# Performance work log

Hardware: AMD Instinct MI355X
Metric: run time of the kernel (lower is better)

The kernel has to match this reference:

```python
import jax, jax.numpy as jnp
import numpy as np

CHANNELS = 10
LENGTH = 64
DEPTH = 4
BATCH = 2048


def setup_inputs() -> dict:
    key = jax.random.key(0)
    x = jax.random.normal(key, (BATCH, CHANNELS * LENGTH), dtype=jnp.float32)
    return {"x": x}


def _seg_exp(dx, depth):
    # Signature of a single linear segment with increment dx: (B, C).
    # Level k is dx^{(x)k} / k! (flattened to (B, C^k)).
    b = dx.shape[0]
    terms = [dx]
    for k in range(2, depth + 1):
        t = jnp.einsum('bi,bj->bij', terms[-1], dx).reshape(b, -1) / k
        terms.append(t)
    return tuple(terms)


def _chen(a, b, depth):
    # Truncated tensor-algebra product (Chen's identity), both with scalar part 1.
    # (A (x) B)_k = A_k + B_k + sum_{i=1}^{k-1} A_i (x) B_{k-i}
    bsz = a[0].shape[0]
    out = []
    for k in range(1, depth + 1):
        t = a[k - 1] + b[k - 1]
        for i in range(1, k):
            t = t + jnp.einsum('bi,bj->bij', a[i - 1], b[k - i - 1]).reshape(bsz, -1)
        out.append(t)
    return tuple(out)


def signature(path, depth):
    # path: (B, C, L). Increments along the path (last) dimension.
    dx = (path[:, :, 1:] - path[:, :, :-1]).transpose(0, 2, 1)  # (B, L-1, C)
    init = _seg_exp(dx[:, 0], depth)

    def step(carry, dxt):
        return _chen(carry, _seg_exp(dxt, depth), depth), None

    sig, _ = jax.lax.scan(step, init, dx[:, 1:].transpose(1, 0, 2))  # scan over L-2 steps
    return jnp.concatenate(sig, axis=-1)  # (B, sum_k C^k)


def reference(x):
    path = x.reshape(x.shape[0], CHANNELS, LENGTH)
    return signature(path, DEPTH)
```

## Files before the change

### kernel.cpp

```cpp
#include <hip/hip_runtime.h>
#include <hip/hip_bf16.h>


typedef short short8 __attribute__((ext_vector_type(8)));
typedef float f2 __attribute__((ext_vector_type(2)));
typedef float f32x4 __attribute__((ext_vector_type(4)));
typedef unsigned int uint4v __attribute__((ext_vector_type(4)));

constexpr int C = 10, L = 64, T = 63;
constexpr int OUTSZ = 10 + 100 + 1000 + 10000;
constexpr int DXP = 11;
constexpr int KS = 64;

__device__ __forceinline__ unsigned packbf(float lo, float hi) {
  union { __hip_bfloat162 h; unsigned u; } cv;
  cv.h = __float22bfloat162_rn(make_float2(lo, hi));
  return cv.u;
}
__device__ __forceinline__ int swz(int row, int k) {
  return row * KS + ((((k >> 3) ^ (row & 7)) << 3) | (k & 7));
}

__global__ __launch_bounds__(512, 6) void sig4_kernel(
    const float* __restrict__ x, float* __restrict__ out)
{
  __shared__ __align__(16) unsigned char smem_raw[45280];
  unsigned short* Ab = (unsigned short*)smem_raw;
  unsigned short* Ub = (unsigned short*)(smem_raw + 12800);
  unsigned short* Bb = (unsigned short*)(smem_raw + 25600);
  float* dxs = (float*)(smem_raw + 39680);
  float* Ps  = (float*)(smem_raw + 42452);

  const int t = threadIdx.x;
  const int w = t >> 6, lane = t & 63;
  const float* __restrict__ xb = x + (size_t)blockIdx.x * (C * L);
  float* __restrict__ ob = out + (size_t)blockIdx.x * OUTSZ;

  for (int i = t; i < T * C; i += 512) {
    int c = i / T, s = i - c * T;
    dxs[s * DXP + c] = xb[c * L + s + 1] - xb[c * L + s];
  }
  __syncthreads();
  for (int c = w; c < C; c += 8) {
    float v = (lane > 0) ? dxs[(lane - 1) * DXP + c] : 0.f;
    #pragma unroll
    for (int d = 1; d < 64; d <<= 1) {
      float y = __shfl_up(v, d);
      if (lane >= d) v += y;
    }
    Ps[lane * DXP + c] = v;
  }
  __syncthreads();

  if (t < 100) {
    const int i_ = t / 10, j_ = t - (t / 10) * 10;
    float s2 = 0.f;
    #pragma unroll
    for (int ch = 0; ch < 8; ++ch) {
      float bu[8], bv[8], zz[8];
      #pragma unroll
      for (int ee = 0; ee < 8; ++ee) {
        const int s = ch * 8 + ee;
        if (s < T) {
          float di = dxs[s * DXP + i_];
          float dj = dxs[s * DXP + j_];
          float p  = Ps[s * DXP + i_];
          bu[ee] = fmaf(di, 0.25f, p) * (dj * (1.f / 3.f));
          bv[ee] = fmaf(di, (1.f / 3.f), p) * (dj * 0.5f);
          zz[ee] = fmaf(di, 0.5f, p) * dj;
        } else { bu[ee] = 0.f; bv[ee] = 0.f; zz[ee] = 0.f; }
      }
      float u2v[8], v2v[8];
      #pragma unroll
      for (int ee = 0; ee < 8; ++ee) {
        u2v[ee] = bu[ee] + s2;
        v2v[ee] = bv[ee] + s2;
        s2 += zz[ee];
      }
      uint4v vp, up;
      #pragma unroll
      for (int q = 0; q < 4; ++q) {
        vp[q] = packbf(v2v[2 * q], v2v[2 * q + 1]);
        up[q] = packbf(u2v[2 * q], u2v[2 * q + 1]);
      }
      *(uint4v*)&Ab[swz(t, ch * 8)] = vp;
      *(uint4v*)&Ub[swz(t, ch * 8)] = up;
    }
    ob[10 + t] = s2;
    if (j_ == 0) ob[i_] = Ps[63 * DXP + i_];
  } else if (t >= 128) {
    const int q = t - 128;
    for (int task = q; task < 110 * 8; task += 384) {
      const int col = task >> 3, ch = task & 7;
      float b1v[8];
      if (col < 100) {
        const int k2 = col / 10, l2 = col - (col / 10) * 10;
        const float S1l = Ps[63 * DXP + l2];
        #pragma unroll
        for (int ee = 0; ee < 8; ++ee) {
          const int kk = ch * 8 + ee;
          b1v[ee] = (kk < T)
              ? dxs[kk * DXP + k2] * (S1l - Ps[(kk + 1) * DXP + l2]) : 0.f;
        }
      } else {
        const int c2 = col - 100;
        #pragma unroll
        for (int ee = 0; ee < 8; ++ee) {
          const int kk = ch * 8 + ee;
          b1v[ee] = (kk < T) ? dxs[kk * DXP + c2] : 0.f;
        }
      }
      uint4v pk;
      #pragma unroll
      for (int qq = 0; qq < 4; ++qq) pk[qq] = packbf(b1v[2 * qq], b1v[2 * qq + 1]);
      *(uint4v*)&Bb[swz(col, ch * 8)] = pk;
    }
  }
  __syncthreads();

  const int lm = lane & 15, lg = lane >> 4;
  f32x4 acc[7];
  #pragma unroll
  for (int ct = 0; ct < 7; ++ct) acc[ct] = f32x4{0.f, 0.f, 0.f, 0.f};

  if (w < 7) {
    const int arow = w * 16 + lm;
    short8 a0 = (arow < 100) ? *(const short8*)&Ab[swz(arow, lg * 8)]
                             : short8{0, 0, 0, 0, 0, 0, 0, 0};
    short8 a1 = (arow < 100) ? *(const short8*)&Ab[swz(arow, 32 + lg * 8)]
                             : short8{0, 0, 0, 0, 0, 0, 0, 0};
    #pragma unroll
    for (int ct = 0; ct < 7; ++ct) {
      const int bcol = ct * 16 + lm;
      short8 b0 = (bcol < 110) ? *(const short8*)&Bb[swz(bcol, lg * 8)]
                               : short8{0, 0, 0, 0, 0, 0, 0, 0};
      short8 b1 = (bcol < 110) ? *(const short8*)&Bb[swz(bcol, 32 + lg * 8)]
                               : short8{0, 0, 0, 0, 0, 0, 0, 0};
      acc[ct] = __builtin_amdgcn_mfma_f32_16x16x32_bf16(b0, a0, acc[ct], 0, 0, 0);
      acc[ct] = __builtin_amdgcn_mfma_f32_16x16x32_bf16(b1, a1, acc[ct], 0, 0, 0);
    }
  }
  __syncthreads();

  for (int task = t; task < 110 * 8; task += 512) {
    const int col = task >> 3, ch = task & 7;
    float b2v[8] = {0.f, 0.f, 0.f, 0.f, 0.f, 0.f, 0.f, 0.f};
    if (col < 100) {
      const int k2 = col / 10, l2 = col - (col / 10) * 10;
      #pragma unroll
      for (int ee = 0; ee < 8; ++ee) {
        const int kk = ch * 8 + ee;
        b2v[ee] = (kk < T) ? dxs[kk * DXP + k2] * dxs[kk * DXP + l2] * 0.5f : 0.f;
      }
    }
    uint4v pk;
    #pragma unroll
    for (int qq = 0; qq < 4; ++qq) pk[qq] = packbf(b2v[2 * qq], b2v[2 * qq + 1]);
    *(uint4v*)&Bb[swz(col, ch * 8)] = pk;
  }
  __syncthreads();

  if (w < 7) {
    const int arow = w * 16 + lm;
    short8 a0 = (arow < 100) ? *(const short8*)&Ub[swz(arow, lg * 8)]
                             : short8{0, 0, 0, 0, 0, 0, 0, 0};
    short8 a1 = (arow < 100) ? *(const short8*)&Ub[swz(arow, 32 + lg * 8)]
                             : short8{0, 0, 0, 0, 0, 0, 0, 0};
    #pragma unroll
    for (int ct = 0; ct < 7; ++ct) {
      const int bcol = ct * 16 + lm;
      short8 b0 = (bcol < 110) ? *(const short8*)&Bb[swz(bcol, lg * 8)]
                               : short8{0, 0, 0, 0, 0, 0, 0, 0};
      short8 b1 = (bcol < 110) ? *(const short8*)&Bb[swz(bcol, 32 + lg * 8)]
                               : short8{0, 0, 0, 0, 0, 0, 0, 0};
      acc[ct] = __builtin_amdgcn_mfma_f32_16x16x32_bf16(b0, a0, acc[ct], 0, 0, 0);
      acc[ct] = __builtin_amdgcn_mfma_f32_16x16x32_bf16(b1, a1, acc[ct], 0, 0, 0);
    }

    const int row = w * 16 + lm;
    if (row < 100) {
      float* rowp4 = ob + 1110 + row * 100;
      float* rowp3 = ob + 110 + row * 10;
      #pragma unroll
      for (int ct = 0; ct < 7; ++ct) {
        const int colbase = ct * 16 + lg * 4;
        f2 lo = {acc[ct][0], acc[ct][1]};
        f2 hi = {acc[ct][2], acc[ct][3]};
        if (colbase < 100) {
          *(f2*)(rowp4 + colbase) = lo;
          *(f2*)(rowp4 + colbase + 2) = hi;
        } else if (colbase < 110) {
          *(f2*)(rowp3 + (colbase - 100)) = lo;
          if (colbase < 108) *(f2*)(rowp3 + (colbase - 98)) = hi;
        }
      }
    }
  }
}

extern "C" void kernel_launch(void* const* d_in, const int* in_sizes, int n_in,
                              void* d_out, int out_size, void* d_ws, size_t ws_size,
                              hipStream_t stream) {
  const float* x = (const float*)d_in[0];
  float* out = (float*)d_out;
  const int batch = in_sizes[0] / (C * L);
  sig4_kernel<<<dim3(batch), dim3(512), 0, stream>>>(x, out);
}
```

Baseline: 35.93 us.

## Parallelize level-2 prefix computation across 8-lane groups with segmented shuffle scan

The serial per-row loop over 64 steps, run by only 100 threads, is split so that each of 8 lanes handles one 8-step chunk. Chunk offsets come from an 8-wide shuffle prefix sum. All 512 threads then share the A/U row building and the B1 column building, where before the threads were split into separate role groups. This shortens the critical path of the setup phase that the MFMA stage waits on, at the cost of extra shuffles and a different floating-point summation order.

```diff
diff --git a/kernel.cpp b/kernel.cpp
--- a/kernel.cpp
+++ b/kernel.cpp
@@ -52,30 +52,40 @@
   }
   __syncthreads();
 
-  if (t < 100) {
-    const int i_ = t / 10, j_ = t - (t / 10) * 10;
-    float s2 = 0.f;
-    #pragma unroll
-    for (int ch = 0; ch < 8; ++ch) {
-      float bu[8], bv[8], zz[8];
-      #pragma unroll
-      for (int ee = 0; ee < 8; ++ee) {
-        const int s = ch * 8 + ee;
+  const int g = lane & 7;
+  #pragma unroll 1
+  for (int it = 0; it < 2; ++it) {
+    const int row = it * 64 + w * 8 + (lane >> 3);
+    if (row < 100) {
+      const int i_ = row / 10, j_ = row - (row / 10) * 10;
+      float z[8], bu[8], bv[8];
+      #pragma unroll
+      for (int e = 0; e < 8; ++e) {
+        const int s = g * 8 + e;
         if (s < T) {
           float di = dxs[s * DXP + i_];
           float dj = dxs[s * DXP + j_];
           float p  = Ps[s * DXP + i_];
-          bu[ee] = fmaf(di, 0.25f, p) * (dj * (1.f / 3.f));
-          bv[ee] = fmaf(di, (1.f / 3.f), p) * (dj * 0.5f);
-          zz[ee] = fmaf(di, 0.5f, p) * dj;
-        } else { bu[ee] = 0.f; bv[ee] = 0.f; zz[ee] = 0.f; }
-      }
+          bu[e] = fmaf(di, 0.25f, p) * (dj * (1.f / 3.f));
+          bv[e] = fmaf(di, (1.f / 3.f), p) * (dj * 0.5f);
+          z[e]  = fmaf(di, 0.5f, p) * dj;
+        } else { bu[e] = 0.f; bv[e] = 0.f; z[e] = 0.f; }
+      }
+      float zsum = ((z[0] + z[1]) + (z[2] + z[3])) +
+                   ((z[4] + z[5]) + (z[6] + z[7]));
+      float a = zsum;
+      #pragma unroll
+      for (int d = 1; d < 8; d <<= 1) {
+        float y = __shfl_up(a, d, 8);
+        if (g >= d) a += y;
+      }
+      float s2 = a - zsum;
       float u2v[8], v2v[8];
       #pragma unroll
-      for (int ee = 0; ee < 8; ++ee) {
-        u2v[ee] = bu[ee] + s2;
-        v2v[ee] = bv[ee] + s2;
-        s2 += zz[ee];
+      for (int e = 0; e < 8; ++e) {
+        u2v[e] = bu[e] + s2;
+        v2v[e] = bv[e] + s2;
+        s2 += z[e];
       }
       uint4v vp, up;
       #pragma unroll
@@ -83,38 +93,37 @@
         vp[q] = packbf(v2v[2 * q], v2v[2 * q + 1]);
         up[q] = packbf(u2v[2 * q], u2v[2 * q + 1]);
       }
-      *(uint4v*)&Ab[swz(t, ch * 8)] = vp;
-      *(uint4v*)&Ub[swz(t, ch * 8)] = up;
-    }
-    ob[10 + t] = s2;
-    if (j_ == 0) ob[i_] = Ps[63 * DXP + i_];
-  } else if (t >= 128) {
-    const int q = t - 128;
-    for (int task = q; task < 110 * 8; task += 384) {
-      const int col = task >> 3, ch = task & 7;
-      float b1v[8];
-      if (col < 100) {
-        const int k2 = col / 10, l2 = col - (col / 10) * 10;
-        const float S1l = Ps[63 * DXP + l2];
-        #pragma unroll
-        for (int ee = 0; ee < 8; ++ee) {
-          const int kk = ch * 8 + ee;
-          b1v[ee] = (kk < T)
-              ? dxs[kk * DXP + k2] * (S1l - Ps[(kk + 1) * DXP + l2]) : 0.f;
-        }
-      } else {
-        const int c2 = col - 100;
-        #pragma unroll
-        for (int ee = 0; ee < 8; ++ee) {
-          const int kk = ch * 8 + ee;
-          b1v[ee] = (kk < T) ? dxs[kk * DXP + c2] : 0.f;
-        }
-      }
-      uint4v pk;
-      #pragma unroll
-      for (int qq = 0; qq < 4; ++qq) pk[qq] = packbf(b1v[2 * qq], b1v[2 * qq + 1]);
-      *(uint4v*)&Bb[swz(col, ch * 8)] = pk;
-    }
+      *(uint4v*)&Ab[swz(row, g * 8)] = vp;
+      *(uint4v*)&Ub[swz(row, g * 8)] = up;
+      if (g == 7) ob[10 + row] = s2;
+    }
+  }
+  if (t < 10) ob[t] = Ps[63 * DXP + t];
+
+  for (int task = t; task < 110 * 8; task += 512) {
+    const int col = task >> 3, ch = task & 7;
+    float b1v[8];
+    if (col < 100) {
+      const int k2 = col / 10, l2 = col - (col / 10) * 10;
+      const float S1l = Ps[63 * DXP + l2];
+      #pragma unroll
+      for (int ee = 0; ee < 8; ++ee) {
+        const int kk = ch * 8 + ee;
+        b1v[ee] = (kk < T)
+            ? dxs[kk * DXP + k2] * (S1l - Ps[(kk + 1) * DXP + l2]) : 0.f;
+      }
+    } else {
+      const int c2 = col - 100;
+      #pragma unroll
+      for (int ee = 0; ee < 8; ++ee) {
+        const int kk = ch * 8 + ee;
+        b1v[ee] = (kk < T) ? dxs[kk * DXP + c2] : 0.f;
+      }
+    }
+    uint4v pk;
+    #pragma unroll
+    for (int qq = 0; qq < 4; ++qq) pk[qq] = packbf(b1v[2 * qq], b1v[2 * qq + 1]);
+    *(uint4v*)&Bb[swz(col, ch * 8)] = pk;
   }
   __syncthreads();
 
```

After: 37.80 us. 5.2% more time.

## Transpose dx and prefix-sum scratch to channel-major padded layout for vector LDS loads

Applied to the files above, without the earlier changes.

Stores the path increments and their prefix sums in shared memory channel-major with a padded stride of 68 and explicit zero padding. The staging loops can then use 128-bit vector LDS reads and drop the per-element bounds checks. This is meant to cut scalar LDS instruction count and branch overhead in the operand-building phases. Vector loads at row strides of 68 floats may cause different bank-conflict patterns.

```diff
diff --git a/kernel.cpp b/kernel.cpp
--- a/kernel.cpp
+++ b/kernel.cpp
@@ -4,12 +4,13 @@
 
 typedef short short8 __attribute__((ext_vector_type(8)));
 typedef float f2 __attribute__((ext_vector_type(2)));
+typedef float f4 __attribute__((ext_vector_type(4)));
 typedef float f32x4 __attribute__((ext_vector_type(4)));
 typedef unsigned int uint4v __attribute__((ext_vector_type(4)));
 
 constexpr int C = 10, L = 64, T = 63;
 constexpr int OUTSZ = 10 + 100 + 1000 + 10000;
-constexpr int DXP = 11;
+constexpr int SP = 68;
 constexpr int KS = 64;
 
 __device__ __forceinline__ unsigned packbf(float lo, float hi) {
@@ -24,58 +25,64 @@
 __global__ __launch_bounds__(512, 6) void sig4_kernel(
     const float* __restrict__ x, float* __restrict__ out)
 {
-  __shared__ __align__(16) unsigned char smem_raw[45280];
+  __shared__ __align__(16) unsigned char smem_raw[45120];
   unsigned short* Ab = (unsigned short*)smem_raw;
   unsigned short* Ub = (unsigned short*)(smem_raw + 12800);
   unsigned short* Bb = (unsigned short*)(smem_raw + 25600);
-  float* dxs = (float*)(smem_raw + 39680);
-  float* Ps  = (float*)(smem_raw + 42452);
+  float* dxT = (float*)(smem_raw + 39680);
+  float* PsT = (float*)(smem_raw + 42400);
 
   const int t = threadIdx.x;
   const int w = t >> 6, lane = t & 63;
   const float* __restrict__ xb = x + (size_t)blockIdx.x * (C * L);
   float* __restrict__ ob = out + (size_t)blockIdx.x * OUTSZ;
 
-  for (int i = t; i < T * C; i += 512) {
-    int c = i / T, s = i - c * T;
-    dxs[s * DXP + c] = xb[c * L + s + 1] - xb[c * L + s];
+  for (int i = t; i < C * SP; i += 512) {
+    int c = i / SP, s = i - c * SP;
+    float v = 0.f;
+    if (s < T) v = xb[c * L + s + 1] - xb[c * L + s];
+    dxT[i] = v;
   }
   __syncthreads();
   for (int c = w; c < C; c += 8) {
-    float v = (lane > 0) ? dxs[(lane - 1) * DXP + c] : 0.f;
+    float v = (lane > 0) ? dxT[c * SP + lane - 1] : 0.f;
     #pragma unroll
     for (int d = 1; d < 64; d <<= 1) {
       float y = __shfl_up(v, d);
       if (lane >= d) v += y;
     }
-    Ps[lane * DXP + c] = v;
-  }
+    PsT[c * SP + lane] = v;
+  }
+  if (t < 40) PsT[(t >> 2) * SP + 64 + (t & 3)] = 0.f;
   __syncthreads();
 
   if (t < 100) {
     const int i_ = t / 10, j_ = t - (t / 10) * 10;
+    const float* dip = dxT + i_ * SP;
+    const float* pp  = PsT + i_ * SP;
+    const float* djp = dxT + j_ * SP;
     float s2 = 0.f;
     #pragma unroll
     for (int ch = 0; ch < 8; ++ch) {
+      f4 d0 = *(const f4*)(dip + ch * 8), d1 = *(const f4*)(dip + ch * 8 + 4);
+      f4 p0 = *(const f4*)(pp  + ch * 8), p1 = *(const f4*)(pp  + ch * 8 + 4);
+      f4 e0 = *(const f4*)(djp + ch * 8), e1 = *(const f4*)(djp + ch * 8 + 4);
+      float di[8] = {d0.x, d0.y, d0.z, d0.w, d1.x, d1.y, d1.z, d1.w};
+      float pv[8] = {p0.x, p0.y, p0.z, p0.w, p1.x, p1.y, p1.z, p1.w};
+      float dj[8] = {e0.x, e0.y, e0.z, e0.w, e1.x, e1.y, e1.z, e1.w};
       float bu[8], bv[8], zz[8];
       #pragma unroll
-      for (int ee = 0; ee < 8; ++ee) {
-        const int s = ch * 8 + ee;
-        if (s < T) {
-          float di = dxs[s * DXP + i_];
-          float dj = dxs[s * DXP + j_];
-          float p  = Ps[s * DXP + i_];
-          bu[ee] = fmaf(di, 0.25f, p) * (dj * (1.f / 3.f));
-          bv[ee] = fmaf(di, (1.f / 3.f), p) * (dj * 0.5f);
-          zz[ee] = fmaf(di, 0.5f, p) * dj;
-        } else { bu[ee] = 0.f; bv[ee] = 0.f; zz[ee] = 0.f; }
+      for (int e = 0; e < 8; ++e) {
+        bu[e] = fmaf(di[e], 0.25f, pv[e]) * (dj[e] * (1.f / 3.f));
+        bv[e] = fmaf(di[e], (1.f / 3.f), pv[e]) * (dj[e] * 0.5f);
+        zz[e] = fmaf(di[e], 0.5f, pv[e]) * dj[e];
       }
       float u2v[8], v2v[8];
       #pragma unroll
-      for (int ee = 0; ee < 8; ++ee) {
-        u2v[ee] = bu[ee] + s2;
-        v2v[ee] = bv[ee] + s2;
-        s2 += zz[ee];
+      for (int e = 0; e < 8; ++e) {
+        u2v[e] = bu[e] + s2;
+        v2v[e] = bv[e] + s2;
+        s2 += zz[e];
       }
       uint4v vp, up;
       #pragma unroll
@@ -87,33 +94,35 @@
       *(uint4v*)&Ub[swz(t, ch * 8)] = up;
     }
     ob[10 + t] = s2;
-    if (j_ == 0) ob[i_] = Ps[63 * DXP + i_];
+    if (j_ == 0) ob[i_] = PsT[i_ * SP + 63];
   } else if (t >= 128) {
     const int q = t - 128;
     for (int task = q; task < 110 * 8; task += 384) {
       const int col = task >> 3, ch = task & 7;
+      const int base = ch * 8;
       float b1v[8];
       if (col < 100) {
         const int k2 = col / 10, l2 = col - (col / 10) * 10;
-        const float S1l = Ps[63 * DXP + l2];
+        const float* dk = dxT + k2 * SP;
+        const float* pl = PsT + l2 * SP;
+        const float S1l = pl[63];
+        f4 d0 = *(const f4*)(dk + base), d1 = *(const f4*)(dk + base + 4);
+        f4 pa = *(const f4*)(pl + base), pb = *(const f4*)(pl + base + 4);
+        f4 pc = *(const f4*)(pl + base + 8);
+        float dv[8] = {d0.x, d0.y, d0.z, d0.w, d1.x, d1.y, d1.z, d1.w};
+        float Pn[8] = {pa.y, pa.z, pa.w, pb.x, pb.y, pb.z, pb.w, pc.x};
         #pragma unroll
-        for (int ee = 0; ee < 8; ++ee) {
-          const int kk = ch * 8 + ee;
-          b1v[ee] = (kk < T)
-              ? dxs[kk * DXP + k2] * (S1l - Ps[(kk + 1) * DXP + l2]) : 0.f;
-        }
+        for (int e = 0; e < 8; ++e) b1v[e] = dv[e] * (S1l - Pn[e]);
       } else {
-        const int c2 = col - 100;
-        #pragma unroll
-        for (int ee = 0; ee < 8; ++ee) {
-          const int kk = ch * 8 + ee;
-          b1v[ee] = (kk < T) ? dxs[kk * DXP + c2] : 0.f;
-        }
+        const float* dk = dxT + (col - 100) * SP;
+        f4 d0 = *(const f4*)(dk + base), d1 = *(const f4*)(dk + base + 4);
+        b1v[0] = d0.x; b1v[1] = d0.y; b1v[2] = d0.z; b1v[3] = d0.w;
+        b1v[4] = d1.x; b1v[5] = d1.y; b1v[6] = d1.z; b1v[7] = d1.w;
       }
       uint4v pk;
       #pragma unroll
       for (int qq = 0; qq < 4; ++qq) pk[qq] = packbf(b1v[2 * qq], b1v[2 * qq + 1]);
-      *(uint4v*)&Bb[swz(col, ch * 8)] = pk;
+      *(uint4v*)&Bb[swz(col, base)] = pk;
     }
   }
   __syncthreads();
@@ -144,19 +153,23 @@
 
   for (int task = t; task < 110 * 8; task += 512) {
     const int col = task >> 3, ch = task & 7;
+    const int base = ch * 8;
     float b2v[8] = {0.f, 0.f, 0.f, 0.f, 0.f, 0.f, 0.f, 0.f};
     if (col < 100) {
       const int k2 = col / 10, l2 = col - (col / 10) * 10;
-      #pragma unroll
-      for (int ee = 0; ee < 8; ++ee) {
-        const int kk = ch * 8 + ee;
-        b2v[ee] = (kk < T) ? dxs[kk * DXP + k2] * dxs[kk * DXP + l2] * 0.5f : 0.f;
-      }
+      const float* dk = dxT + k2 * SP;
+      const float* dl = dxT + l2 * SP;
+      f4 a0 = *(const f4*)(dk + base), a1 = *(const f4*)(dk + base + 4);
+      f4 c0 = *(const f4*)(dl + base), c1 = *(const f4*)(dl + base + 4);
+      b2v[0] = a0.x * c0.x * 0.5f; b2v[1] = a0.y * c0.y * 0.5f;
+      b2v[2] = a0.z * c0.z * 0.5f; b2v[3] = a0.w * c0.w * 0.5f;
+      b2v[4] = a1.x * c1.x * 0.5f; b2v[5] = a1.y * c1.y * 0.5f;
+      b2v[6] = a1.z * c1.z * 0.5f; b2v[7] = a1.w * c1.w * 0.5f;
     }
     uint4v pk;
     #pragma unroll
     for (int qq = 0; qq < 4; ++qq) pk[qq] = packbf(b2v[2 * qq], b2v[2 * qq + 1]);
-    *(uint4v*)&Bb[swz(col, ch * 8)] = pk;
+    *(uint4v*)&Bb[swz(col, base)] = pk;
   }
   __syncthreads();
 
```

Measured after the change: 33.83 us. 1.06x faster.
